# Kernel tuning notes

Hardware: AMD Instinct MI355X
Metric: run time of the kernel (lower is better)

Reference implementation:

```python
import jax, jax.numpy as jnp
import numpy as np


def setup_inputs() -> dict:
    key = jax.random.key(0)
    k1, k2 = jax.random.split(key)
    token_inputs = jax.random.normal(k1, (4, 2048, 4096), dtype=jnp.float32)
    w_gate = jax.random.normal(k2, (4096, 64), dtype=jnp.float32)
    return {"token_inputs": token_inputs, "w_gate": w_gate, "expert_capacity": 40}


def reference(token_inputs, w_gate, expert_capacity):
    # Gating: [b, n, d] @ [d, e] -> [b, n, e]
    router_logits = jnp.einsum('bnd,de->bne', token_inputs, w_gate)

    # Router z-loss: mean of squared logsumexp over experts.
    z_loss = jnp.mean(jax.nn.logsumexp(router_logits, axis=-1) ** 2)

    router_probs = jax.nn.softmax(router_logits, axis=-1)
    num_experts = router_probs.shape[-1]

    # Top-1 (Switch) routing.
    expert_index = jnp.argmax(router_probs, axis=-1)          # [b, n]
    expert_gate = jnp.max(router_probs, axis=-1)              # [b, n]
    expert_mask = jax.nn.one_hot(expert_index, num_experts,
                                 dtype=router_probs.dtype)    # [b, n, e]

    # Load-balancing auxiliary loss.
    density = jnp.mean(expert_mask, axis=1)                   # [b, e] dispatch fraction
    density_proxy = jnp.mean(router_probs, axis=1)            # [b, e] mean prob
    aux_loss = jnp.mean(density * density_proxy) * (num_experts ** 2)

    # Capacity assignment via cumulative sum over tokens (0-based slot index).
    position_in_expert = (jnp.cumsum(expert_mask, axis=1) - 1.0) * expert_mask  # [b, n, e]
    within_capacity = (position_in_expert < expert_capacity).astype(router_probs.dtype) * expert_mask

    pos_idx = position_in_expert.astype(jnp.int32)            # [b, n, e]
    # Dispatch: one-hot over capacity slots, zeroed for dropped tokens. [b, n, e, c]
    dispatch_tensor = within_capacity[..., None] * jax.nn.one_hot(
        pos_idx, expert_capacity, dtype=router_probs.dtype)
    # Combine: dispatch scaled by the router gate probability.
    combine_tensor = dispatch_tensor * expert_gate[:, :, None, None]

    return dispatch_tensor, combine_tensor, aux_loss, z_loss
```

## Files before the change

### kernel.cpp

```cpp
#include <hip/hip_runtime.h>
#include <stdint.h>

#define B_    4
#define N_    2048
#define D_    4096
#define E_    64
#define TOKENS (B_ * N_)
#define KT    32
#define TM    64
#define KS    8
#define KCHUNK (D_ / KS)

typedef float vfloat4 __attribute__((ext_vector_type(4)));

__global__ __launch_bounds__(256) void k_gemm_z(const float* __restrict__ A,
                                                const float* __restrict__ W,
                                                float* __restrict__ P,
                                                float* __restrict__ out,
                                                float* __restrict__ probsum,
                                                float* __restrict__ losses) {
    __shared__ float As[KT][TM + 4];
    __shared__ float Ws[KT][E_ + 4];

    const int tid   = threadIdx.x;
    const int tok0  = blockIdx.x * TM;
    const int kc    = blockIdx.y;
    const int kbase = kc * KCHUNK;
    const int blin  = kc * gridDim.x + blockIdx.x;

    const int t0 = (tid >> 4) * 4;
    const int e0 = (tid & 15) * 4;

    const int a_kf = (tid & 7) * 4;
    const int a_t  = tid >> 3;
    const int w_e  = (tid & 15) * 4;
    const int w_k  = tid >> 4;

    vfloat4* zbase = reinterpret_cast<vfloat4*>(out) + (size_t)blin * 10240 + tid;
    int zstep = 0;
    const vfloat4 z4 = {0.f, 0.f, 0.f, 0.f};

    if (blin == 0) {
        if (tid < B_ * E_) probsum[tid] = 0.f;
        if (tid < 2)       losses[tid]  = 0.f;
    }

    float acc[4][4] = {{0.f}};

    #pragma unroll 1
    for (int kt = 0; kt < KCHUNK; kt += KT) {
        const float* gA = A + (size_t)tok0 * D_ + (size_t)(kbase + kt);
        #pragma unroll
        for (int it = 0; it < 2; ++it) {
            const int tok = a_t + it * 32;
            const float4 v = *reinterpret_cast<const float4*>(
                gA + (size_t)tok * D_ + a_kf);
            As[a_kf + 0][tok] = v.x;
            As[a_kf + 1][tok] = v.y;
            As[a_kf + 2][tok] = v.z;
            As[a_kf + 3][tok] = v.w;
        }
        const float* gW = W + (size_t)(kbase + kt) * E_;
        #pragma unroll
        for (int it = 0; it < 2; ++it) {
            const int kk = w_k + it * 16;
            const float4 v = *reinterpret_cast<const float4*>(gW + kk * E_ + w_e);
            *reinterpret_cast<float4*>(&Ws[kk][w_e]) = v;
        }
        __syncthreads();

        {
            const int nz = (kt < 8 * KT) ? 3 : 2;
            for (int j = 0; j < nz; ++j) {
                __builtin_nontemporal_store(z4, zbase + (size_t)zstep * 256);
                ++zstep;
            }
        }

        #pragma unroll
        for (int kk = 0; kk < KT; ++kk) {
            const float4 a = *reinterpret_cast<const float4*>(&As[kk][t0]);
            const float4 b = *reinterpret_cast<const float4*>(&Ws[kk][e0]);
            acc[0][0] += a.x * b.x; acc[0][1] += a.x * b.y;
            acc[0][2] += a.x * b.z; acc[0][3] += a.x * b.w;
            acc[1][0] += a.y * b.x; acc[1][1] += a.y * b.y;
            acc[1][2] += a.y * b.z; acc[1][3] += a.y * b.w;
            acc[2][0] += a.z * b.x; acc[2][1] += a.z * b.y;
            acc[2][2] += a.z * b.z; acc[2][3] += a.z * b.w;
            acc[3][0] += a.w * b.x; acc[3][1] += a.w * b.y;
            acc[3][2] += a.w * b.z; acc[3][3] += a.w * b.w;
        }
        __syncthreads();
    }

    float* base = P + ((size_t)kc * TOKENS + tok0) * E_;
    #pragma unroll
    for (int i = 0; i < 4; ++i) {
        const float4 v = make_float4(acc[i][0], acc[i][1], acc[i][2], acc[i][3]);
        *reinterpret_cast<float4*>(&base[(size_t)(t0 + i) * E_ + e0]) = v;
    }
}

__global__ __launch_bounds__(256) void k_softmax(const float* __restrict__ P,
                                                 int* __restrict__ idx,
                                                 float* __restrict__ gate,
                                                 float* __restrict__ probsum,
                                                 float* __restrict__ out_z) {
    const int tid  = threadIdx.x;
    const int wid  = tid >> 6;
    const int lane = tid & 63;
    const int tok  = blockIdx.x * 4 + wid;

    float l = 0.f;
    #pragma unroll
    for (int kc = 0; kc < KS; ++kc)
        l += P[((size_t)kc * TOKENS + tok) * E_ + lane];

    float m = l; int mi = lane;
    #pragma unroll
    for (int off = 32; off > 0; off >>= 1) {
        const float om = __shfl_down(m, off);
        const int   oi = __shfl_down(mi, off);
        if (om > m || (om == m && oi < mi)) { m = om; mi = oi; }
    }
    m  = __shfl(m, 0);
    mi = __shfl(mi, 0);

    const float p = __expf(l - m);
    float s = p;
    #pragma unroll
    for (int off = 32; off > 0; off >>= 1) s += __shfl_down(s, off);
    s = __shfl(s, 0);

    __shared__ float pacc[4][E_];
    __shared__ float zv[4];
    pacc[wid][lane] = p / s;
    if (lane == 0) {
        const float lse = m + logf(s);
        zv[wid]   = lse * lse;
        idx[tok]  = mi;
        gate[tok] = 1.0f / s;
    }
    __syncthreads();

    if (tid < E_) {
        const float ps = pacc[0][tid] + pacc[1][tid] + pacc[2][tid] + pacc[3][tid];
        const int b = (blockIdx.x * 4) / N_;
        atomicAdd(&probsum[b * E_ + tid], ps);
    }
    if (tid == 0)
        atomicAdd(out_z, (zv[0] + zv[1] + zv[2] + zv[3]) * (1.0f / (float)TOKENS));
}

__global__ __launch_bounds__(64) void k_posloss(const int* __restrict__ idx,
                                                const float* __restrict__ gate,
                                                const float* __restrict__ probsum,
                                                float* __restrict__ out,
                                                float* __restrict__ out_aux,
                                                int C, size_t half) {
    const int b = blockIdx.x >> 6;
    const int e = blockIdx.x & 63;
    const int lane = threadIdx.x;
    const int*   ib = idx  + b * N_;
    const float* gb = gate + b * N_;
    float* ob = out + (size_t)b * N_ * E_ * C;

    int running = 0;
    for (int step = 0; step < N_ / 64; ++step) {
        const int t = step * 64 + lane;
        const bool match = (ib[t] == e);
        const unsigned long long mask = __ballot(match);
        if (match) {
            const int p = running + __popcll(mask & ((1ull << lane) - 1ull));
            if (p < C) {
                const size_t off = (size_t)t * E_ * C + (size_t)e * C + p;
                ob[off] = 1.0f;
                ob[half + off] = gb[t];
            }
        }
        running += __popcll(mask);
    }
    if (lane == 0)
        atomicAdd(out_aux,
                  (float)running * probsum[b * E_ + e] * (1.0f / 262144.0f));
}

extern "C" void kernel_launch(void* const* d_in, const int* in_sizes, int n_in,
                              void* d_out, int out_size, void* d_ws, size_t ws_size,
                              hipStream_t stream) {
    const float* A = (const float*)d_in[0];
    const float* W = (const float*)d_in[1];
    float* out = (float*)d_out;

    const size_t half = ((size_t)out_size - 2) / 2;
    const int C = (int)(half / ((size_t)TOKENS * E_));

    float* P = (float*)d_ws;
    size_t off = (size_t)KS * TOKENS * E_;
    int*   idx     = (int*)(P + off);   off += TOKENS;
    float* gate    = P + off;           off += TOKENS;
    float* probsum = P + off;           off += B_ * E_;

    float* out_aux = out + 2 * half;
    float* out_z   = out + 2 * half + 1;

    k_gemm_z<<<dim3(TOKENS / TM, KS), 256, 0, stream>>>(A, W, P, out, probsum,
                                                        out_aux);
    k_softmax<<<TOKENS / 4, 256, 0, stream>>>(P, idx, gate, probsum, out_z);
    k_posloss<<<B_ * E_, 64, 0, stream>>>(idx, gate, probsum, out, out_aux, C, half);
}
```

Before: 331.3 us.

## Enlarge GEMM token tile, deepen split-K, and prefetch next tiles into registers

Each block of the gating GEMM now covers 128 tokens and each thread holds an 8x4 accumulator tile. The K dimension is split 16 ways with 16-wide k-steps. The global loads for the next k-step are issued into registers before the current tile is computed, so load latency overlaps with the FMAs. The aim is more arithmetic per shared-memory read and better hiding of memory latency. In exchange, the softmax kernel now reduces 16 partial sums per logit instead of 8, which doubles the partial-sum workspace and the traffic to read it back.

```diff
diff --git a/kernel.cpp b/kernel.cpp
--- a/kernel.cpp
+++ b/kernel.cpp
@@ -6,10 +6,13 @@
 #define D_    4096
 #define E_    64
 #define TOKENS (B_ * N_)
-#define KT    32
-#define TM    64
-#define KS    8
+#define KT    16
+#define TM    128
+#define KS    16
 #define KCHUNK (D_ / KS)
+#define NIT   (KCHUNK / KT)
+#define PA    (TM + 4)
+#define PW    (E_ + 4)
 
 typedef float vfloat4 __attribute__((ext_vector_type(4)));
 
@@ -19,8 +22,8 @@
                                                 float* __restrict__ out,
                                                 float* __restrict__ probsum,
                                                 float* __restrict__ losses) {
-    __shared__ float As[KT][TM + 4];
-    __shared__ float Ws[KT][E_ + 4];
+    __shared__ float As[KT][PA];
+    __shared__ float Ws[KT][PW];
 
     const int tid   = threadIdx.x;
     const int tok0  = blockIdx.x * TM;
@@ -28,49 +31,53 @@
     const int kbase = kc * KCHUNK;
     const int blin  = kc * gridDim.x + blockIdx.x;
 
-    const int t0 = (tid >> 4) * 4;
-    const int e0 = (tid & 15) * 4;
-
-    const int a_kf = (tid & 7) * 4;
-    const int a_t  = tid >> 3;
-    const int w_e  = (tid & 15) * 4;
-    const int w_k  = tid >> 4;
+    const int t0 = (tid & 15) * 8;
+    const int e0 = (tid >> 4) * 4;
+
+    const int a_k = (tid & 3) * 4;
+    const int a_t = tid >> 2;
+    const int w_k = tid >> 4;
+    const int w_e = (tid & 15) * 4;
 
     vfloat4* zbase = reinterpret_cast<vfloat4*>(out) + (size_t)blin * 10240 + tid;
     int zstep = 0;
     const vfloat4 z4 = {0.f, 0.f, 0.f, 0.f};
 
     if (blin == 0) {
-        if (tid < B_ * E_) probsum[tid] = 0.f;
-        if (tid < 2)       losses[tid]  = 0.f;
-    }
-
-    float acc[4][4] = {{0.f}};
+        probsum[tid] = 0.f;
+        if (tid < 2) losses[tid] = 0.f;
+    }
+
+    const float* gA = A + (size_t)tok0 * D_ + kbase;
+
+    float4 pa0 = *reinterpret_cast<const float4*>(gA + (size_t)a_t * D_ + a_k);
+    float4 pa1 = *reinterpret_cast<const float4*>(gA + (size_t)(a_t + 64) * D_ + a_k);
+    float4 pw  = *reinterpret_cast<const float4*>(W + (size_t)(kbase + w_k) * E_ + w_e);
+
+    float acc[8][4] = {{0.f}};
 
     #pragma unroll 1
-    for (int kt = 0; kt < KCHUNK; kt += KT) {
-        const float* gA = A + (size_t)tok0 * D_ + (size_t)(kbase + kt);
-        #pragma unroll
-        for (int it = 0; it < 2; ++it) {
-            const int tok = a_t + it * 32;
-            const float4 v = *reinterpret_cast<const float4*>(
-                gA + (size_t)tok * D_ + a_kf);
-            As[a_kf + 0][tok] = v.x;
-            As[a_kf + 1][tok] = v.y;
-            As[a_kf + 2][tok] = v.z;
-            As[a_kf + 3][tok] = v.w;
-        }
-        const float* gW = W + (size_t)(kbase + kt) * E_;
-        #pragma unroll
-        for (int it = 0; it < 2; ++it) {
-            const int kk = w_k + it * 16;
-            const float4 v = *reinterpret_cast<const float4*>(gW + kk * E_ + w_e);
-            *reinterpret_cast<float4*>(&Ws[kk][w_e]) = v;
-        }
+    for (int it = 0; it < NIT; ++it) {
+        As[a_k + 0][a_t]      = pa0.x;
+        As[a_k + 1][a_t]      = pa0.y;
+        As[a_k + 2][a_t]      = pa0.z;
+        As[a_k + 3][a_t]      = pa0.w;
+        As[a_k + 0][a_t + 64] = pa1.x;
+        As[a_k + 1][a_t + 64] = pa1.y;
+        As[a_k + 2][a_t + 64] = pa1.z;
+        As[a_k + 3][a_t + 64] = pa1.w;
+        *reinterpret_cast<float4*>(&Ws[w_k][w_e]) = pw;
         __syncthreads();
 
+        if (it + 1 < NIT) {
+            const int ko = (it + 1) * KT;
+            pa0 = *reinterpret_cast<const float4*>(gA + (size_t)a_t * D_ + ko + a_k);
+            pa1 = *reinterpret_cast<const float4*>(gA + (size_t)(a_t + 64) * D_ + ko + a_k);
+            pw  = *reinterpret_cast<const float4*>(W + (size_t)(kbase + ko + w_k) * E_ + w_e);
+        }
+
         {
-            const int nz = (kt < 8 * KT) ? 3 : 2;
+            const int nz = (it < 8) ? 3 : 2;
             for (int j = 0; j < nz; ++j) {
                 __builtin_nontemporal_store(z4, zbase + (size_t)zstep * 256);
                 ++zstep;
@@ -79,23 +86,22 @@
 
         #pragma unroll
         for (int kk = 0; kk < KT; ++kk) {
-            const float4 a = *reinterpret_cast<const float4*>(&As[kk][t0]);
-            const float4 b = *reinterpret_cast<const float4*>(&Ws[kk][e0]);
-            acc[0][0] += a.x * b.x; acc[0][1] += a.x * b.y;
-            acc[0][2] += a.x * b.z; acc[0][3] += a.x * b.w;
-            acc[1][0] += a.y * b.x; acc[1][1] += a.y * b.y;
-            acc[1][2] += a.y * b.z; acc[1][3] += a.y * b.w;
-            acc[2][0] += a.z * b.x; acc[2][1] += a.z * b.y;
-            acc[2][2] += a.z * b.z; acc[2][3] += a.z * b.w;
-            acc[3][0] += a.w * b.x; acc[3][1] += a.w * b.y;
-            acc[3][2] += a.w * b.z; acc[3][3] += a.w * b.w;
+            float a[8], b[4];
+            *reinterpret_cast<float4*>(&a[0]) = *reinterpret_cast<const float4*>(&As[kk][t0]);
+            *reinterpret_cast<float4*>(&a[4]) = *reinterpret_cast<const float4*>(&As[kk][t0 + 4]);
+            *reinterpret_cast<float4*>(&b[0]) = *reinterpret_cast<const float4*>(&Ws[kk][e0]);
+            #pragma unroll
+            for (int i = 0; i < 8; ++i)
+                #pragma unroll
+                for (int j = 0; j < 4; ++j)
+                    acc[i][j] += a[i] * b[j];
         }
         __syncthreads();
     }
 
     float* base = P + ((size_t)kc * TOKENS + tok0) * E_;
     #pragma unroll
-    for (int i = 0; i < 4; ++i) {
+    for (int i = 0; i < 8; ++i) {
         const float4 v = make_float4(acc[i][0], acc[i][1], acc[i][2], acc[i][3]);
         *reinterpret_cast<float4*>(&base[(size_t)(t0 + i) * E_ + e0]) = v;
     }
```

Measured after the change: 339.0 us. 1.02x slower.
